# Optimization experiments

Hardware: AMD Instinct MI355X
Metric: run time of the kernel (lower is better)

The kernel has to match this reference:

```python
import jax, jax.numpy as jnp
import numpy as np

N = 50000   # nodes per graph
E = 800000  # edges per graph
D = 128     # in_dim (num_features)
H = 128     # hidden_channels
R = 8       # num_etypes


def setup_inputs() -> dict:
    key = jax.random.key(0)
    ks = jax.random.split(key, 32)
    inp = {}
    inp["x1"] = jax.random.normal(ks[0], (N, D), dtype=jnp.float32)
    inp["edge_index1"] = jax.random.randint(ks[1], (2, E), 0, N)
    inp["edge_type1"] = jnp.sort(jax.random.randint(ks[2], (E,), 0, R))
    inp["x2"] = jax.random.normal(ks[3], (N, D), dtype=jnp.float32)
    inp["edge_index2"] = jax.random.randint(ks[4], (2, E), 0, N)
    inp["edge_type2"] = jnp.sort(jax.random.randint(ks[5], (E,), 0, R))
    # RGCNConv params: relation weights [R, in, out], root weight [in, out], bias [out]
    dims = [(D, H), (H, H), (H, H)]
    k = 6
    for l, (di, do) in enumerate(dims):
        s = 1.0 / np.sqrt(di)
        inp[f"W{l}"] = jax.random.normal(ks[k], (R, di, do), dtype=jnp.float32) * s; k += 1
        inp[f"root{l}"] = jax.random.normal(ks[k], (di, do), dtype=jnp.float32) * s; k += 1
        inp[f"bias{l}"] = jnp.zeros((do,), dtype=jnp.float32)
    # FCL: MLP on concat(u1, u2) of width 2*H -> H -> 1 (assumed architecture)
    s = 1.0 / np.sqrt(2 * H)
    inp["fc1_w"] = jax.random.normal(ks[k], (2 * H, H), dtype=jnp.float32) * s; k += 1
    inp["fc1_b"] = jnp.zeros((H,), dtype=jnp.float32)
    s = 1.0 / np.sqrt(H)
    inp["fc2_w"] = jax.random.normal(ks[k], (H, 1), dtype=jnp.float32) * s; k += 1
    inp["fc2_b"] = jnp.zeros((1,), dtype=jnp.float32)
    return inp


def rgcn_conv(x, src, dst, etype, W, root, bias):
    # PyG RGCNConv: out_i = root @ x_i + bias + sum_r mean_{j in N_r(i)} W_r x_j
    # transform all nodes by all relation weights: [R, N, H]
    t = jnp.einsum('nd,rdh->rnh', x, W)
    msg = t[etype, src]                       # [E, H] per-edge gathered messages
    comb = dst * R + etype                    # combined (node, relation) segment id
    cnt = jax.ops.segment_sum(jnp.ones((E,), x.dtype), comb, num_segments=N * R)
    msg = msg * (1.0 / jnp.maximum(cnt, 1.0))[comb][:, None]  # per-relation mean norm
    agg = jax.ops.segment_sum(msg, dst, num_segments=N)       # scatter-add over relations
    return agg + x @ root + bias


def gnn(x, edge_index, edge_type, params):
    src, dst = edge_index[0], edge_index[1]
    u = jax.nn.relu(rgcn_conv(x, src, dst, edge_type, *params[0]))
    u = jax.nn.relu(rgcn_conv(u, src, dst, edge_type, *params[1]))
    u = rgcn_conv(u, src, dst, edge_type, *params[2])
    return jnp.mean(u, axis=0).reshape(1, -1)  # [1, H]


def reference(x1, edge_index1, edge_type1, x2, edge_index2, edge_type2,
              W0, root0, bias0, W1, root1, bias1, W2, root2, bias2,
              fc1_w, fc1_b, fc2_w, fc2_b):
    params = [(W0, root0, bias0), (W1, root1, bias1), (W2, root2, bias2)]
    u1 = gnn(x1, edge_index1, edge_type1, params)
    u2 = gnn(x2, edge_index2, edge_type2, params)
    h = jnp.concatenate([u1, u2], axis=-1)    # [1, 2H]
    return jax.nn.relu(h @ fc1_w + fc1_b) @ fc2_w + fc2_b  # [1, 1]
```

## Files before the change

### kernel.cpp

```cpp
#include <hip/hip_runtime.h>

#define R_ET 8
#define DH 128

typedef __bf16 bf16x8 __attribute__((ext_vector_type(8)));
typedef float f32x4 __attribute__((ext_vector_type(4)));

__device__ __forceinline__ ushort f2bf(float f) {
  unsigned u = __float_as_uint(f);
  u += 0x7fff + ((u >> 16) & 1);
  return (ushort)(u >> 16);
}

__global__ void count_kernel(const int* __restrict__ ei, const int* __restrict__ et,
                             int* __restrict__ cnt, int E) {
  int e = blockIdx.x * blockDim.x + threadIdx.x;
  if (e < E) atomicAdd(&cnt[ei[E + e] * R_ET + et[e]], 1);
}

__global__ __launch_bounds__(1024) void scan1_kernel(const int* __restrict__ cnt,
                                                     int* __restrict__ off,
                                                     int* __restrict__ bsum, int N) {
  __shared__ int s[1024];
  int tid = threadIdx.x;
  int node = blockIdx.x * 1024 + tid;
  int d = 0;
  if (node < N) {
    const int4* c = (const int4*)&cnt[node * R_ET];
    int4 a = c[0], b = c[1];
    d = a.x + a.y + a.z + a.w + b.x + b.y + b.z + b.w;
  }
  s[tid] = d;
  __syncthreads();
  for (int step = 1; step < 1024; step <<= 1) {
    int v = (tid >= step) ? s[tid - step] : 0;
    __syncthreads();
    s[tid] += v;
    __syncthreads();
  }
  if (node < N) off[node] = s[tid] - d;
  if (tid == 1023) bsum[blockIdx.x] = s[1023];
}

__global__ __launch_bounds__(1024) void scan2_kernel(int* __restrict__ bsum, int nb) {
  __shared__ int s[1024];
  int tid = threadIdx.x;
  int v = (tid < nb) ? bsum[tid] : 0;
  s[tid] = v;
  __syncthreads();
  for (int step = 1; step < 1024; step <<= 1) {
    int x = (tid >= step) ? s[tid - step] : 0;
    __syncthreads();
    s[tid] += x;
    __syncthreads();
  }
  if (tid < nb) bsum[tid] = s[tid] - v;
}

__global__ __launch_bounds__(1024) void scan3_kernel(int* __restrict__ off,
                                                     int* __restrict__ cursor,
                                                     const int* __restrict__ bsum,
                                                     int N, int E) {
  int node = blockIdx.x * 1024 + threadIdx.x;
  if (node < N) {
    int o = off[node] + bsum[blockIdx.x];
    off[node] = o;
    cursor[node] = o;
  }
  if (node == 0) off[N] = E;
}

__global__ void place_kernel(const int* __restrict__ ei, const int* __restrict__ et,
                             const int* __restrict__ cnt, int* __restrict__ cursor,
                             int* __restrict__ sorted, float* __restrict__ scale, int E) {
  int e = blockIdx.x * blockDim.x + threadIdx.x;
  if (e >= E) return;
  int src = ei[e], dst = ei[E + e], r = et[e];
  int slot = atomicAdd(&cursor[dst], 1);
  sorted[slot] = src | (r << 28);
  scale[slot] = 1.f / (float)cnt[dst * R_ET + r];
}

__global__ __launch_bounds__(256) void wconv_kernel(const float* __restrict__ root,
                                                    const float* __restrict__ W,
                                                    ushort* __restrict__ Wt) {
  int mat = blockIdx.x;
  const float* src = (mat == 0) ? root : (W + (size_t)(mat - 1) * DH * DH);
  ushort* dst = Wt + (size_t)mat * DH * DH;
  for (int idx = threadIdx.x; idx < DH * DH; idx += 256) {
    int n = idx >> 7, k = idx & 127;
    dst[idx] = f2bf(src[k * DH + n]);
  }
}

__global__ __launch_bounds__(256) void aconv_kernel(const float* __restrict__ src,
                                                    ushort* __restrict__ dst,
                                                    int total, int padtotal) {
  int i4 = (blockIdx.x * 256 + threadIdx.x) * 4;
  if (i4 >= padtotal) return;
  ushort4 o = make_ushort4(0, 0, 0, 0);
  if (i4 < total) {
    float4 v = *(const float4*)&src[i4];
    o = make_ushort4(f2bf(v.x), f2bf(v.y), f2bf(v.z), f2bf(v.w));
  }
  *(ushort4*)&dst[i4] = o;
}

__global__ __launch_bounds__(256) void gemm_mfma(
    const ushort* __restrict__ Abf, const ushort* __restrict__ Wt,
    const float* __restrict__ bias, float* __restrict__ y,
    ushort* __restrict__ t, int N) {
  __shared__ ushort As[128 * 32];
  __shared__ ushort Bs[128 * 32];
  const int tid = threadIdx.x;
  const int wave = tid >> 6, lane = tid & 63;
  const int quad = lane >> 4, l15 = lane & 15;
  const int cb = blockIdx.y;
  const int rbase = blockIdx.x * 128;
  const ushort* gB = Wt + (size_t)cb * (DH * DH);
  const int wr = (wave >> 1) * 64, wc = (wave & 1) * 64;

  f32x4 acc[4][4];
#pragma unroll
  for (int i = 0; i < 4; i++)
#pragma unroll
    for (int j = 0; j < 4; j++) acc[i][j] = (f32x4){0.f, 0.f, 0.f, 0.f};

  for (int kc = 0; kc < 4; kc++) {
    if (kc) __syncthreads();
#pragma unroll
    for (int it = 0; it < 2; it++) {
      int piece = it * 256 + tid;
      int row = piece >> 2, sub = piece & 3;
      const ushort* ga = Abf + ((size_t)(rbase + row) * DH + kc * 32 + sub * 8);
      const ushort* gb = gB + ((size_t)row * DH + kc * 32 + sub * 8);
      ushort* la = As + (size_t)(it * 256 + wave * 64) * 8;
      ushort* lb = Bs + (size_t)(it * 256 + wave * 64) * 8;
      __builtin_amdgcn_global_load_lds((const __attribute__((address_space(1))) void*)ga,
                                       (__attribute__((address_space(3))) void*)la, 16, 0, 0);
      __builtin_amdgcn_global_load_lds((const __attribute__((address_space(1))) void*)gb,
                                       (__attribute__((address_space(3))) void*)lb, 16, 0, 0);
    }
    __syncthreads();
    bf16x8 af[4], bfr[4];
#pragma unroll
    for (int i = 0; i < 4; i++) {
      af[i] = *(const bf16x8*)&As[(wr + i * 16 + l15) * 32 + quad * 8];
      bfr[i] = *(const bf16x8*)&Bs[(wc + i * 16 + l15) * 32 + quad * 8];
    }
#pragma unroll
    for (int i = 0; i < 4; i++)
#pragma unroll
      for (int j = 0; j < 4; j++)
        acc[i][j] = __builtin_amdgcn_mfma_f32_16x16x32_bf16(af[i], bfr[j], acc[i][j], 0, 0, 0);
  }

  if (cb == 0) {
#pragma unroll
    for (int j = 0; j < 4; j++) {
      int col = wc + j * 16 + l15;
      float bv = bias[col];
#pragma unroll
      for (int i = 0; i < 4; i++)
#pragma unroll
        for (int r = 0; r < 4; r++) {
          int row = rbase + wr + i * 16 + quad * 4 + r;
          if (row < N) y[(size_t)row * DH + col] = acc[i][j][r] + bv;
        }
    }
  } else {
    ushort* tp = t + (size_t)(cb - 1) * N * DH;
#pragma unroll
    for (int j = 0; j < 4; j++) {
      int col = wc + j * 16 + l15;
#pragma unroll
      for (int i = 0; i < 4; i++)
#pragma unroll
        for (int r = 0; r < 4; r++) {
          int row = rbase + wr + i * 16 + quad * 4 + r;
          if (row < N) tp[(size_t)row * DH + col] = f2bf(acc[i][j][r]);
        }
    }
  }
}

__global__ __launch_bounds__(256) void gather_mid(
    const int* __restrict__ off, const int* __restrict__ sorted,
    const float* __restrict__ scale, const ushort* __restrict__ t,
    const float* __restrict__ y, ushort* __restrict__ Abf, int N) {
  int dst = blockIdx.x * 4 + (threadIdx.x >> 6);
  if (dst >= N) return;
  int lane = threadIdx.x & 63;
  int start = off[dst], end = off[dst + 1];
  float ax = 0.f, ay = 0.f;
  for (int base = start; base < end; base += 64) {
    int m = min(64, end - base);
    int p = 0;
    float s = 0.f;
    if (lane < m) { p = sorted[base + lane]; s = scale[base + lane]; }
    for (int j = 0; j < m; j++) {
      int pj = __shfl(p, j);
      float sj = __shfl(s, j);
      int src = pj & 0x0fffffff, r = pj >> 28;
      unsigned u = *(const unsigned*)&t[((size_t)r * N + src) * DH + lane * 2];
      ax = fmaf(__uint_as_float(u << 16), sj, ax);
      ay = fmaf(__uint_as_float(u & 0xffff0000u), sj, ay);
    }
  }
  float2 yv = *(const float2*)&y[(size_t)dst * DH + lane * 2];
  float rx = fmaxf(yv.x + ax, 0.f);
  float ry = fmaxf(yv.y + ay, 0.f);
  unsigned o = (unsigned)f2bf(rx) | ((unsigned)f2bf(ry) << 16);
  *(unsigned*)&Abf[(size_t)dst * DH + lane * 2] = o;
}

__global__ __launch_bounds__(256) void gather_last(
    const int* __restrict__ off, const int* __restrict__ sorted,
    const float* __restrict__ scale, const ushort* __restrict__ t,
    float* __restrict__ y, int N) {
  int dst = blockIdx.x * 4 + (threadIdx.x >> 6);
  if (dst >= N) return;
  int lane = threadIdx.x & 63;
  int start = off[dst], end = off[dst + 1];
  float ax = 0.f, ay = 0.f;
  for (int base = start; base < end; base += 64) {
    int m = min(64, end - base);
    int p = 0;
    float s = 0.f;
    if (lane < m) { p = sorted[base + lane]; s = scale[base + lane]; }
    for (int j = 0; j < m; j++) {
      int pj = __shfl(p, j);
      float sj = __shfl(s, j);
      int src = pj & 0x0fffffff, r = pj >> 28;
      unsigned u = *(const unsigned*)&t[((size_t)r * N + src) * DH + lane * 2];
      ax = fmaf(__uint_as_float(u << 16), sj, ax);
      ay = fmaf(__uint_as_float(u & 0xffff0000u), sj, ay);
    }
  }
  float2* yp = (float2*)&y[(size_t)dst * DH + lane * 2];
  float2 yv = *yp;
  yv.x += ax;
  yv.y += ay;
  *yp = yv;
}

__global__ __launch_bounds__(256) void pool_kernel(const float* __restrict__ y,
                                                   float* __restrict__ u, int N) {
  __shared__ float s[256];
  int tid = threadIdx.x;
  int c = tid & 127, rr = tid >> 7;
  int n0 = blockIdx.x * 100;
  int nend = min(n0 + 100, N);
  float sum = 0.f;
  for (int n = n0 + rr; n < nend; n += 2) sum += y[(size_t)n * DH + c];
  s[tid] = sum;
  __syncthreads();
  if (tid < 128) atomicAdd(&u[c], s[tid] + s[tid + 128]);
}

__global__ __launch_bounds__(256) void mlp_kernel(
    const float* __restrict__ u, const float* __restrict__ fc1w,
    const float* __restrict__ fc1b, const float* __restrict__ fc2w,
    const float* __restrict__ fc2b, float* __restrict__ out, int N) {
  __shared__ float uin[256];
  __shared__ float hred[128];
  int tid = threadIdx.x;
  uin[tid] = u[tid] * (1.f / (float)N);
  __syncthreads();
  if (tid < 128) {
    float s = fc1b[tid];
    for (int i = 0; i < 256; i++) s = fmaf(uin[i], fc1w[i * 128 + tid], s);
    s = fmaxf(s, 0.f);
    hred[tid] = s * fc2w[tid];
  }
  __syncthreads();
  if (tid == 0) {
    float s = fc2b[0];
    for (int i = 0; i < 128; i++) s += hred[i];
    out[0] = s;
  }
}

extern "C" void kernel_launch(void* const* d_in, const int* in_sizes, int n_in,
                              void* d_out, int out_size, void* d_ws, size_t ws_size,
                              hipStream_t stream) {
  const float* x[2] = {(const float*)d_in[0], (const float*)d_in[3]};
  const int* ei[2] = {(const int*)d_in[1], (const int*)d_in[4]};
  const int* et[2] = {(const int*)d_in[2], (const int*)d_in[5]};
  const float* Wp[3] = {(const float*)d_in[6], (const float*)d_in[9], (const float*)d_in[12]};
  const float* rootp[3] = {(const float*)d_in[7], (const float*)d_in[10], (const float*)d_in[13]};
  const float* biasp[3] = {(const float*)d_in[8], (const float*)d_in[11], (const float*)d_in[14]};
  const float* fc1w = (const float*)d_in[15];
  const float* fc1b = (const float*)d_in[16];
  const float* fc2w = (const float*)d_in[17];
  const float* fc2b = (const float*)d_in[18];

  const int N = in_sizes[0] / DH;
  const int E = in_sizes[2];
  const int Npad = (N + 127) & ~127;
  const int NB = (N + 1023) / 1024;

  char* ws = (char*)d_ws;
  size_t ob = 0;
  auto alloc = [&](size_t bytes) {
    void* p = ws + ob;
    ob = (ob + bytes + 255) & ~(size_t)255;
    return p;
  };
  float* y = (float*)alloc((size_t)N * DH * 4);
  int* cnt = (int*)alloc((size_t)N * R_ET * 4);
  int* offs = (int*)alloc((size_t)(N + 1) * 4);
  int* cursor = (int*)alloc((size_t)N * 4);
  int* bsum = (int*)alloc(1024 * 4);
  int* sorted = (int*)alloc((size_t)E * 4);
  float* scale = (float*)alloc((size_t)E * 4);
  float* u = (float*)alloc(1024);
  ushort* Abf = (ushort*)alloc((size_t)Npad * DH * 2);
  ushort* Wt = (ushort*)alloc((size_t)3 * 9 * DH * DH * 2);
  ushort* tbuf = (ushort*)alloc((size_t)R_ET * N * DH * 2);
  (void)ws_size;

  hipMemsetAsync(u, 0, 2 * DH * sizeof(float), stream);
  for (int l = 0; l < 3; l++)
    wconv_kernel<<<9, 256, 0, stream>>>(rootp[l], Wp[l], Wt + (size_t)l * 9 * DH * DH);

  dim3 ggrid(Npad / 128, R_ET + 1);
  dim3 egrid((E + 255) / 256);
  dim3 ngrid((N + 3) / 4);
  const int total = N * DH, padtotal = Npad * DH;
  dim3 agrid((padtotal / 4 + 255) / 256);

  for (int g = 0; g < 2; g++) {
    hipMemsetAsync(cnt, 0, (size_t)N * R_ET * sizeof(int), stream);
    count_kernel<<<egrid, 256, 0, stream>>>(ei[g], et[g], cnt, E);
    scan1_kernel<<<NB, 1024, 0, stream>>>(cnt, offs, bsum, N);
    scan2_kernel<<<1, 1024, 0, stream>>>(bsum, NB);
    scan3_kernel<<<NB, 1024, 0, stream>>>(offs, cursor, bsum, N, E);
    place_kernel<<<egrid, 256, 0, stream>>>(ei[g], et[g], cnt, cursor, sorted, scale, E);
    aconv_kernel<<<agrid, 256, 0, stream>>>(x[g], Abf, total, padtotal);
    for (int l = 0; l < 3; l++) {
      gemm_mfma<<<ggrid, 256, 0, stream>>>(Abf, Wt + (size_t)l * 9 * DH * DH,
                                           biasp[l], y, tbuf, N);
      if (l < 2) {
        gather_mid<<<ngrid, 256, 0, stream>>>(offs, sorted, scale, tbuf, y, Abf, N);
      } else {
        gather_last<<<ngrid, 256, 0, stream>>>(offs, sorted, scale, tbuf, y, N);
      }
    }
    pool_kernel<<<(N + 99) / 100, 256, 0, stream>>>(y, u + g * DH, N);
  }
  mlp_kernel<<<1, 256, 0, stream>>>(u, fc1w, fc1b, fc2w, fc2b, (float*)d_out, N);
}
```

Measured before the change: 1.052 ms.

## Reuse full A tile across three weight matrices, swizzle LDS, pack edge metadata

The GEMM now loads the whole 128x128 A tile into LDS once and loops over three weight matrices per block, so the grid's y dimension shrinks from 9 to 3 and A is re-fetched far less often. A and W are stored in global memory with an XOR swizzle on their 8-element chunks, which avoids LDS bank conflicts when fragments are read. Edge source/type and scale are packed into one int2 array, and the gather loop is unrolled by 4 so more loads are in flight. The larger LDS footprint (64KB per block) may lower occupancy, and the swizzled layout has to stay consistent across aconv, gather_mid and wconv.

```diff
diff --git a/kernel.cpp b/kernel.cpp
--- a/kernel.cpp
+++ b/kernel.cpp
@@ -11,6 +11,7 @@
   u += 0x7fff + ((u >> 16) & 1);
   return (ushort)(u >> 16);
 }
+
 
 __global__ void count_kernel(const int* __restrict__ ei, const int* __restrict__ et,
                              int* __restrict__ cnt, int E) {
@@ -72,13 +73,13 @@
 
 __global__ void place_kernel(const int* __restrict__ ei, const int* __restrict__ et,
                              const int* __restrict__ cnt, int* __restrict__ cursor,
-                             int* __restrict__ sorted, float* __restrict__ scale, int E) {
+                             int2* __restrict__ meta, int E) {
   int e = blockIdx.x * blockDim.x + threadIdx.x;
   if (e >= E) return;
   int src = ei[e], dst = ei[E + e], r = et[e];
   int slot = atomicAdd(&cursor[dst], 1);
-  sorted[slot] = src | (r << 28);
-  scale[slot] = 1.f / (float)cnt[dst * R_ET + r];
+  meta[slot] = make_int2(src | (r << 28),
+                         __float_as_int(1.f / (float)cnt[dst * R_ET + r]));
 }
 
 __global__ __launch_bounds__(256) void wconv_kernel(const float* __restrict__ root,
@@ -89,7 +90,7 @@
   ushort* dst = Wt + (size_t)mat * DH * DH;
   for (int idx = threadIdx.x; idx < DH * DH; idx += 256) {
     int n = idx >> 7, k = idx & 127;
-    dst[idx] = f2bf(src[k * DH + n]);
+    dst[n * DH + (((k >> 3) ^ (n & 7)) << 3) + (k & 7)] = f2bf(src[k * DH + n]);
   }
 }
 
@@ -98,145 +99,165 @@
                                                     int total, int padtotal) {
   int i4 = (blockIdx.x * 256 + threadIdx.x) * 4;
   if (i4 >= padtotal) return;
+  int row = i4 >> 7, k = i4 & 127;
   ushort4 o = make_ushort4(0, 0, 0, 0);
   if (i4 < total) {
     float4 v = *(const float4*)&src[i4];
     o = make_ushort4(f2bf(v.x), f2bf(v.y), f2bf(v.z), f2bf(v.w));
   }
-  *(ushort4*)&dst[i4] = o;
+  *(ushort4*)&dst[(size_t)row * DH + (((k >> 3) ^ (row & 7)) << 3) + (k & 7)] = o;
 }
 
 __global__ __launch_bounds__(256) void gemm_mfma(
     const ushort* __restrict__ Abf, const ushort* __restrict__ Wt,
     const float* __restrict__ bias, float* __restrict__ y,
     ushort* __restrict__ t, int N) {
-  __shared__ ushort As[128 * 32];
-  __shared__ ushort Bs[128 * 32];
+  __shared__ ushort As[128 * DH];
+  __shared__ ushort Bs[128 * DH];
   const int tid = threadIdx.x;
   const int wave = tid >> 6, lane = tid & 63;
   const int quad = lane >> 4, l15 = lane & 15;
-  const int cb = blockIdx.y;
   const int rbase = blockIdx.x * 128;
-  const ushort* gB = Wt + (size_t)cb * (DH * DH);
   const int wr = (wave >> 1) * 64, wc = (wave & 1) * 64;
 
-  f32x4 acc[4][4];
-#pragma unroll
-  for (int i = 0; i < 4; i++)
-#pragma unroll
-    for (int j = 0; j < 4; j++) acc[i][j] = (f32x4){0.f, 0.f, 0.f, 0.f};
-
-  for (int kc = 0; kc < 4; kc++) {
-    if (kc) __syncthreads();
-#pragma unroll
-    for (int it = 0; it < 2; it++) {
-      int piece = it * 256 + tid;
-      int row = piece >> 2, sub = piece & 3;
-      const ushort* ga = Abf + ((size_t)(rbase + row) * DH + kc * 32 + sub * 8);
-      const ushort* gb = gB + ((size_t)row * DH + kc * 32 + sub * 8);
-      ushort* la = As + (size_t)(it * 256 + wave * 64) * 8;
-      ushort* lb = Bs + (size_t)(it * 256 + wave * 64) * 8;
-      __builtin_amdgcn_global_load_lds((const __attribute__((address_space(1))) void*)ga,
-                                       (__attribute__((address_space(3))) void*)la, 16, 0, 0);
-      __builtin_amdgcn_global_load_lds((const __attribute__((address_space(1))) void*)gb,
-                                       (__attribute__((address_space(3))) void*)lb, 16, 0, 0);
-    }
-    __syncthreads();
-    bf16x8 af[4], bfr[4];
-#pragma unroll
-    for (int i = 0; i < 4; i++) {
-      af[i] = *(const bf16x8*)&As[(wr + i * 16 + l15) * 32 + quad * 8];
-      bfr[i] = *(const bf16x8*)&Bs[(wc + i * 16 + l15) * 32 + quad * 8];
-    }
+  const ushort* gA = Abf + (size_t)rbase * DH;
+#pragma unroll
+  for (int it = 0; it < 8; it++) {
+    __builtin_amdgcn_global_load_lds(
+        (const __attribute__((address_space(1))) void*)(gA + (it * 256 + tid) * 8),
+        (__attribute__((address_space(3))) void*)(As + (it * 256 + wave * 64) * 8), 16, 0, 0);
+  }
+
+  for (int m = 0; m < 3; m++) {
+    const int mat = blockIdx.y * 3 + m;
+    const ushort* gB = Wt + (size_t)mat * DH * DH;
+    if (m) __syncthreads();
+#pragma unroll
+    for (int it = 0; it < 8; it++) {
+      __builtin_amdgcn_global_load_lds(
+          (const __attribute__((address_space(1))) void*)(gB + (it * 256 + tid) * 8),
+          (__attribute__((address_space(3))) void*)(Bs + (it * 256 + wave * 64) * 8), 16, 0, 0);
+    }
+    __syncthreads();
+
+    f32x4 acc[4][4];
 #pragma unroll
     for (int i = 0; i < 4; i++)
 #pragma unroll
-      for (int j = 0; j < 4; j++)
-        acc[i][j] = __builtin_amdgcn_mfma_f32_16x16x32_bf16(af[i], bfr[j], acc[i][j], 0, 0, 0);
-  }
-
-  if (cb == 0) {
-#pragma unroll
-    for (int j = 0; j < 4; j++) {
-      int col = wc + j * 16 + l15;
-      float bv = bias[col];
+      for (int j = 0; j < 4; j++) acc[i][j] = (f32x4){0.f, 0.f, 0.f, 0.f};
+
+#pragma unroll
+    for (int kc = 0; kc < 4; kc++) {
+      bf16x8 af[4], bfr[4];
+#pragma unroll
+      for (int i = 0; i < 4; i++) {
+        int ra = wr + i * 16 + l15;
+        int rb = wc + i * 16 + l15;
+        af[i] = *(const bf16x8*)&As[ra * DH + (((kc * 4 + quad) ^ (ra & 7)) << 3)];
+        bfr[i] = *(const bf16x8*)&Bs[rb * DH + (((kc * 4 + quad) ^ (rb & 7)) << 3)];
+      }
 #pragma unroll
       for (int i = 0; i < 4; i++)
 #pragma unroll
-        for (int r = 0; r < 4; r++) {
-          int row = rbase + wr + i * 16 + quad * 4 + r;
-          if (row < N) y[(size_t)row * DH + col] = acc[i][j][r] + bv;
-        }
-    }
-  } else {
-    ushort* tp = t + (size_t)(cb - 1) * N * DH;
-#pragma unroll
-    for (int j = 0; j < 4; j++) {
-      int col = wc + j * 16 + l15;
-#pragma unroll
-      for (int i = 0; i < 4; i++)
-#pragma unroll
-        for (int r = 0; r < 4; r++) {
-          int row = rbase + wr + i * 16 + quad * 4 + r;
-          if (row < N) tp[(size_t)row * DH + col] = f2bf(acc[i][j][r]);
-        }
+        for (int j = 0; j < 4; j++)
+          acc[i][j] = __builtin_amdgcn_mfma_f32_16x16x32_bf16(af[i], bfr[j], acc[i][j], 0, 0, 0);
+    }
+
+    if (mat == 0) {
+#pragma unroll
+      for (int j = 0; j < 4; j++) {
+        int col = wc + j * 16 + l15;
+        float bv = bias[col];
+#pragma unroll
+        for (int i = 0; i < 4; i++)
+#pragma unroll
+          for (int r = 0; r < 4; r++) {
+            int row = rbase + wr + i * 16 + quad * 4 + r;
+            if (row < N) y[(size_t)row * DH + col] = acc[i][j][r] + bv;
+          }
+      }
+    } else {
+      ushort* tp = t + (size_t)(mat - 1) * N * DH;
+#pragma unroll
+      for (int j = 0; j < 4; j++) {
+        int col = wc + j * 16 + l15;
+#pragma unroll
+        for (int i = 0; i < 4; i++)
+#pragma unroll
+          for (int r = 0; r < 4; r++) {
+            int row = rbase + wr + i * 16 + quad * 4 + r;
+            if (row < N) tp[(size_t)row * DH + col] = f2bf(acc[i][j][r]);
+          }
+      }
+    }
+  }
+}
+
+__device__ __forceinline__ void gather_accum(const int2* __restrict__ meta,
+                                             const ushort* __restrict__ t,
+                                             int start, int end, int lane, int N,
+                                             float& ax, float& ay) {
+  const int colb = lane * 2;
+  for (int base = start; base < end; base += 64) {
+    int m = min(64, end - base);
+    int2 md = make_int2(0, 0);
+    if (lane < m) md = meta[base + lane];
+    int j = 0;
+    for (; j + 4 <= m; j += 4) {
+      int p0 = __shfl(md.x, j),     q0 = __shfl(md.y, j);
+      int p1 = __shfl(md.x, j + 1), q1 = __shfl(md.y, j + 1);
+      int p2 = __shfl(md.x, j + 2), q2 = __shfl(md.y, j + 2);
+      int p3 = __shfl(md.x, j + 3), q3 = __shfl(md.y, j + 3);
+      unsigned u0 = *(const unsigned*)&t[(((size_t)((unsigned)p0 >> 28) * N + (p0 & 0x0fffffff)) << 7) + colb];
+      unsigned u1 = *(const unsigned*)&t[(((size_t)((unsigned)p1 >> 28) * N + (p1 & 0x0fffffff)) << 7) + colb];
+      unsigned u2 = *(const unsigned*)&t[(((size_t)((unsigned)p2 >> 28) * N + (p2 & 0x0fffffff)) << 7) + colb];
+      unsigned u3 = *(const unsigned*)&t[(((size_t)((unsigned)p3 >> 28) * N + (p3 & 0x0fffffff)) << 7) + colb];
+      float s0 = __int_as_float(q0), s1 = __int_as_float(q1);
+      float s2 = __int_as_float(q2), s3 = __int_as_float(q3);
+      ax = fmaf(__uint_as_float(u0 << 16), s0, ax);
+      ay = fmaf(__uint_as_float(u0 & 0xffff0000u), s0, ay);
+      ax = fmaf(__uint_as_float(u1 << 16), s1, ax);
+      ay = fmaf(__uint_as_float(u1 & 0xffff0000u), s1, ay);
+      ax = fmaf(__uint_as_float(u2 << 16), s2, ax);
+      ay = fmaf(__uint_as_float(u2 & 0xffff0000u), s2, ay);
+      ax = fmaf(__uint_as_float(u3 << 16), s3, ax);
+      ay = fmaf(__uint_as_float(u3 & 0xffff0000u), s3, ay);
+    }
+    for (; j < m; j++) {
+      int pj = __shfl(md.x, j);
+      float sj = __int_as_float(__shfl(md.y, j));
+      unsigned u = *(const unsigned*)&t[(((size_t)((unsigned)pj >> 28) * N + (pj & 0x0fffffff)) << 7) + colb];
+      ax = fmaf(__uint_as_float(u << 16), sj, ax);
+      ay = fmaf(__uint_as_float(u & 0xffff0000u), sj, ay);
     }
   }
 }
 
 __global__ __launch_bounds__(256) void gather_mid(
-    const int* __restrict__ off, const int* __restrict__ sorted,
-    const float* __restrict__ scale, const ushort* __restrict__ t,
-    const float* __restrict__ y, ushort* __restrict__ Abf, int N) {
+    const int* __restrict__ off, const int2* __restrict__ meta,
+    const ushort* __restrict__ t, const float* __restrict__ y,
+    ushort* __restrict__ Abf, int N) {
   int dst = blockIdx.x * 4 + (threadIdx.x >> 6);
   if (dst >= N) return;
   int lane = threadIdx.x & 63;
-  int start = off[dst], end = off[dst + 1];
   float ax = 0.f, ay = 0.f;
-  for (int base = start; base < end; base += 64) {
-    int m = min(64, end - base);
-    int p = 0;
-    float s = 0.f;
-    if (lane < m) { p = sorted[base + lane]; s = scale[base + lane]; }
-    for (int j = 0; j < m; j++) {
-      int pj = __shfl(p, j);
-      float sj = __shfl(s, j);
-      int src = pj & 0x0fffffff, r = pj >> 28;
-      unsigned u = *(const unsigned*)&t[((size_t)r * N + src) * DH + lane * 2];
-      ax = fmaf(__uint_as_float(u << 16), sj, ax);
-      ay = fmaf(__uint_as_float(u & 0xffff0000u), sj, ay);
-    }
-  }
+  gather_accum(meta, t, off[dst], off[dst + 1], lane, N, ax, ay);
   float2 yv = *(const float2*)&y[(size_t)dst * DH + lane * 2];
   float rx = fmaxf(yv.x + ax, 0.f);
   float ry = fmaxf(yv.y + ay, 0.f);
   unsigned o = (unsigned)f2bf(rx) | ((unsigned)f2bf(ry) << 16);
-  *(unsigned*)&Abf[(size_t)dst * DH + lane * 2] = o;
+  int k = lane * 2;
+  *(unsigned*)&Abf[(size_t)dst * DH + (((k >> 3) ^ (dst & 7)) << 3) + (k & 7)] = o;
 }
 
 __global__ __launch_bounds__(256) void gather_last(
-    const int* __restrict__ off, const int* __restrict__ sorted,
-    const float* __restrict__ scale, const ushort* __restrict__ t,
-    float* __restrict__ y, int N) {
+    const int* __restrict__ off, const int2* __restrict__ meta,
+    const ushort* __restrict__ t, float* __restrict__ y, int N) {
   int dst = blockIdx.x * 4 + (threadIdx.x >> 6);
   if (dst >= N) return;
   int lane = threadIdx.x & 63;
-  int start = off[dst], end = off[dst + 1];
   float ax = 0.f, ay = 0.f;
-  for (int base = start; base < end; base += 64) {
-    int m = min(64, end - base);
-    int p = 0;
-    float s = 0.f;
-    if (lane < m) { p = sorted[base + lane]; s = scale[base + lane]; }
-    for (int j = 0; j < m; j++) {
-      int pj = __shfl(p, j);
-      float sj = __shfl(s, j);
-      int src = pj & 0x0fffffff, r = pj >> 28;
-      unsigned u = *(const unsigned*)&t[((size_t)r * N + src) * DH + lane * 2];
-      ax = fmaf(__uint_as_float(u << 16), sj, ax);
-      ay = fmaf(__uint_as_float(u & 0xffff0000u), sj, ay);
-    }
-  }
+  gather_accum(meta, t, off[dst], off[dst + 1], lane, N, ax, ay);
   float2* yp = (float2*)&y[(size_t)dst * DH + lane * 2];
   float2 yv = *yp;
   yv.x += ax;
@@ -312,8 +333,7 @@
   int* offs = (int*)alloc((size_t)(N + 1) * 4);
   int* cursor = (int*)alloc((size_t)N * 4);
   int* bsum = (int*)alloc(1024 * 4);
-  int* sorted = (int*)alloc((size_t)E * 4);
-  float* scale = (float*)alloc((size_t)E * 4);
+  int2* meta = (int2*)alloc((size_t)E * 8);
   float* u = (float*)alloc(1024);
   ushort* Abf = (ushort*)alloc((size_t)Npad * DH * 2);
   ushort* Wt = (ushort*)alloc((size_t)3 * 9 * DH * DH * 2);
@@ -324,7 +344,7 @@
   for (int l = 0; l < 3; l++)
     wconv_kernel<<<9, 256, 0, stream>>>(rootp[l], Wp[l], Wt + (size_t)l * 9 * DH * DH);
 
-  dim3 ggrid(Npad / 128, R_ET + 1);
+  dim3 ggrid(Npad / 128, 3);
   dim3 egrid((E + 255) / 256);
   dim3 ngrid((N + 3) / 4);
   const int total = N * DH, padtotal = Npad * DH;
@@ -336,15 +356,15 @@
     scan1_kernel<<<NB, 1024, 0, stream>>>(cnt, offs, bsum, N);
     scan2_kernel<<<1, 1024, 0, stream>>>(bsum, NB);
     scan3_kernel<<<NB, 1024, 0, stream>>>(offs, cursor, bsum, N, E);
-    place_kernel<<<egrid, 256, 0, stream>>>(ei[g], et[g], cnt, cursor, sorted, scale, E);
+    place_kernel<<<egrid, 256, 0, stream>>>(ei[g], et[g], cnt, cursor, meta, E);
     aconv_kernel<<<agrid, 256, 0, stream>>>(x[g], Abf, total, padtotal);
     for (int l = 0; l < 3; l++) {
       gemm_mfma<<<ggrid, 256, 0, stream>>>(Abf, Wt + (size_t)l * 9 * DH * DH,
                                            biasp[l], y, tbuf, N);
       if (l < 2) {
-        gather_mid<<<ngrid, 256, 0, stream>>>(offs, sorted, scale, tbuf, y, Abf, N);
+        gather_mid<<<ngrid, 256, 0, stream>>>(offs, meta, tbuf, y, Abf, N);
       } else {
-        gather_last<<<ngrid, 256, 0, stream>>>(offs, sorted, scale, tbuf, y, N);
+        gather_last<<<ngrid, 256, 0, stream>>>(offs, meta, tbuf, y, N);
       }
     }
     pool_kernel<<<(N + 99) / 100, 256, 0, stream>>>(y, u + g * DH, N);
```

Result: faster. 887.6 us (-15.6%).
